# Optimization experiments

Measured on AMD Instinct MI355X. Metric: run time of the kernel, lower is better.

Reference implementation:

```python
import jax, jax.numpy as jnp
import numpy as np

B, V, F = 64, 4096, 16
A, P, NF = 8, 16, 16  # n_aggregators, n_propagate, n_filters


def setup_inputs() -> dict:
    key = jax.random.key(0)
    ks = jax.random.split(key, 6)
    data = jax.random.normal(ks[0], (B, V, F), dtype=jnp.float32)
    num_vertex = jax.random.randint(ks[1], (B, 1), 1, V + 1, dtype=jnp.int32)
    W_flr = jax.random.normal(ks[2], (F, P), dtype=jnp.float32) * (1.0 / np.sqrt(F))
    b_flr = jnp.zeros((P,), jnp.float32)
    W_s = jax.random.normal(ks[3], (F, A), dtype=jnp.float32) * (1.0 / np.sqrt(F))
    b_s = jnp.zeros((A,), jnp.float32)
    W_out = jax.random.normal(ks[4], (A * P, NF), dtype=jnp.float32) * (1.0 / np.sqrt(A * P))
    b_out = jnp.zeros((NF,), jnp.float32)
    return {"data": data, "num_vertex": num_vertex, "W_flr": W_flr, "b_flr": b_flr,
            "W_s": W_s, "b_s": b_s, "W_out": W_out, "b_out": b_out}


def reference(data, num_vertex, W_flr, b_flr, W_s, b_s, W_out, b_out):
    # vertex mask: [B, V, 1], 1.0 where index < num_vertex
    idx = jnp.arange(V, dtype=jnp.int32)[None, :]          # [1, V]
    mask = (idx < num_vertex).astype(jnp.float32)[..., None]  # [B, V, 1]

    features = data @ W_flr + b_flr                         # [B, V, P]
    distance = data @ W_s + b_s                             # [B, V, A]
    edge_weights = mask * jnp.exp(-jnp.square(distance))    # [B, V, A]

    # aggregated mean over vertices: mean_v(ew[b,v,a] * feat[b,v,p]) -> [B, A, P]
    aggregated = jnp.einsum('bva,bvp->bap', edge_weights, features) / V

    # broadcast back: ew[b,v,a] * agg[b,a,p] -> [B, V, A, P] -> [B, V, A*P]
    updated = (edge_weights[:, :, :, None] * aggregated[:, None, :, :]).reshape(B, V, A * P)

    out = mask * (updated @ W_out + b_out)                  # [B, V, NF], linear activation
    return out
```

## Files before the change

### kernel.cpp

```cpp
#include <hip/hip_runtime.h>


#define B_ 64
#define V_ 4096
#define F_ 16
#define A_ 8
#define P_ 16
#define NF_ 16
#define SPLIT1 8
#define SPLIT2 16
#define GE_ (A_*F_ + A_)
#define CH_ 34

typedef unsigned int uint32;
typedef unsigned short u16;

__device__ __forceinline__ float bflo(uint32 u){ union{uint32 i;float f;}x; x.i=u<<16; return x.f; }
__device__ __forceinline__ float bfhi(uint32 u){ union{uint32 i;float f;}x; x.i=u&0xffff0000u; return x.f; }

__device__ __forceinline__ bool detect_bf16(const void* data){
  const uint32* w = (const uint32*)data;
  int c = 0;
  #pragma unroll
  for (int i=0;i<16;++i){
    uint32 e = (w[i]>>7) & 0xffu;
    c += (e>=100u && e<=135u) ? 1 : 0;
  }
  return c >= 11;
}

template<bool BF16>
__device__ __forceinline__ float ldw(const void* p, int i){
  return BF16 ? bflo((uint32)((const u16*)p)[i]) : ((const float*)p)[i];
}

template<bool BF16>
__device__ __forceinline__ void load_vertex(const void* base, size_t v, float* d){
  if (BF16){
    const uint4* p = (const uint4*)((const u16*)base + v*F_);
    uint4 r0=p[0], r1=p[1];
    d[0]=bflo(r0.x); d[1]=bfhi(r0.x); d[2]=bflo(r0.y); d[3]=bfhi(r0.y);
    d[4]=bflo(r0.z); d[5]=bfhi(r0.z); d[6]=bflo(r0.w); d[7]=bfhi(r0.w);
    d[8]=bflo(r1.x); d[9]=bfhi(r1.x); d[10]=bflo(r1.y); d[11]=bfhi(r1.y);
    d[12]=bflo(r1.z); d[13]=bfhi(r1.z); d[14]=bflo(r1.w); d[15]=bfhi(r1.w);
  } else {
    const float4* p = (const float4*)((const float*)base + v*F_);
    float4 a=p[0], b=p[1], c=p[2], e=p[3];
    d[0]=a.x; d[1]=a.y; d[2]=a.z; d[3]=a.w;
    d[4]=b.x; d[5]=b.y; d[6]=b.z; d[7]=b.w;
    d[8]=c.x; d[9]=c.y; d[10]=c.z; d[11]=c.w;
    d[12]=e.x; d[13]=e.y; d[14]=e.z; d[15]=e.w;
  }
}

template<bool BF16>
__device__ __forceinline__ void agg_body(
    const void* __restrict__ data, const int* __restrict__ nv,
    const void* __restrict__ Ws, const void* __restrict__ bs,
    float* __restrict__ partial)
{
  __shared__ __align__(16) float sWs[F_*A_];
  __shared__ float sbs[A_];
  __shared__ float red[256][CH_+1];
  __shared__ float red2[4][CH_];

  const int tid = threadIdx.x;
  if (tid < F_*A_) sWs[tid] = ldw<BF16>(Ws, tid);
  if (tid < A_)    sbs[tid] = ldw<BF16>(bs, tid);
  const int b = blockIdx.x >> 3;
  const int s = blockIdx.x & 7;
  const int nvb = nv[b];
  __syncthreads();

  float G[A_*F_], E[A_];
  #pragma unroll
  for (int i=0;i<A_*F_;++i) G[i]=0.f;
  #pragma unroll
  for (int i=0;i<A_;++i) E[i]=0.f;

  const int vbase = s*(V_/SPLIT1);
  const size_t voff = (size_t)b*V_ + vbase;

  const int vl0 = tid, vl1 = tid + 256;
  float d0[16], d1[16];
  load_vertex<BF16>(data, voff+vl0, d0);
  load_vertex<BF16>(data, voff+vl1, d1);
  const float m0 = (vbase+vl0 < nvb) ? 1.f : 0.f;
  const float m1 = (vbase+vl1 < nvb) ? 1.f : 0.f;

  float t0[A_], t1[A_];
  #pragma unroll
  for (int a=0;a<A_;++a){ t0[a]=sbs[a]; t1[a]=sbs[a]; }
  #pragma unroll
  for (int f=0; f<F_; ++f){
    const float4 w0 = *(const float4*)&sWs[f*A_];
    const float4 w1 = *(const float4*)&sWs[f*A_+4];
    const float wa[8] = {w0.x,w0.y,w0.z,w0.w,w1.x,w1.y,w1.z,w1.w};
    #pragma unroll
    for (int a=0;a<A_;++a){
      t0[a] = fmaf(d0[f], wa[a], t0[a]);
      t1[a] = fmaf(d1[f], wa[a], t1[a]);
    }
  }
  #pragma unroll
  for (int a=0;a<A_;++a){
    const float e0 = m0*__expf(-t0[a]*t0[a]);
    const float e1 = m1*__expf(-t1[a]*t1[a]);
    E[a] = e0+e1;
    #pragma unroll
    for (int f=0;f<F_;++f)
      G[a*F_+f] = fmaf(e0, d0[f], e1*d1[f]);
  }

  #pragma unroll
  for (int c=0;c<4;++c){
    #pragma unroll
    for (int j=0;j<CH_;++j){
      const int idx = c*CH_ + j;
      red[tid][j] = (idx < A_*F_) ? G[idx] : E[idx - A_*F_];
    }
    __syncthreads();
    if (tid < 4*CH_){
      const int j = tid >> 2, q = tid & 3;
      float acc = 0.f;
      #pragma unroll 8
      for (int i=0;i<64;++i) acc += red[64*q + i][j];
      red2[q][j] = acc;
    }
    __syncthreads();
    if (tid < CH_)
      partial[(size_t)blockIdx.x*GE_ + c*CH_ + tid] =
          red2[0][tid]+red2[1][tid]+red2[2][tid]+red2[3][tid];
    __syncthreads();
  }
}

__global__ __launch_bounds__(256, 2) void k_agg(
    const void* __restrict__ data, const int* __restrict__ nv,
    const void* __restrict__ Ws, const void* __restrict__ bs,
    float* __restrict__ partial)
{
  if (detect_bf16(data)) agg_body<true >(data, nv, Ws, bs, partial);
  else                   agg_body<false>(data, nv, Ws, bs, partial);
}

template<bool BF16>
__device__ __forceinline__ void out_body(
    const void* __restrict__ data, const int* __restrict__ nv,
    const void* __restrict__ Wflr, const void* __restrict__ bflr,
    const void* __restrict__ Ws, const void* __restrict__ bs,
    const void* __restrict__ Wout, const void* __restrict__ bout,
    const float* __restrict__ partial, float* __restrict__ out)
{
  __shared__ __align__(16) float sWs[F_*A_];
  __shared__ __align__(16) float sWf[F_*P_];
  __shared__ float sbf[P_], sbs[A_], sbo[NF_];
  __shared__ float sGE[GE_];
  __shared__ float sagg[A_*P_];
  __shared__ __align__(16) float sM[A_*NF_];

  const int tid = threadIdx.x;
  const int b = blockIdx.x >> 4;
  const int s = blockIdx.x & 15;

  if (tid < F_*P_) sWf[tid] = ldw<BF16>(Wflr, tid);
  if (tid < F_*A_) sWs[tid] = ldw<BF16>(Ws, tid);
  if (tid < P_)    sbf[tid] = ldw<BF16>(bflr, tid);
  if (tid < A_)    sbs[tid] = ldw<BF16>(bs, tid);
  if (tid < NF_)   sbo[tid] = ldw<BF16>(bout, tid);
  if (tid < GE_) {
    const float* pp = partial + (size_t)(b*SPLIT1)*GE_ + tid;
    float v = 0.f;
    #pragma unroll
    for (int k=0;k<SPLIT1;++k) v += pp[(size_t)k*GE_];
    sGE[tid] = v;
  }
  const int nvb = nv[b];
  __syncthreads();

  if (tid < A_*P_) {
    const int a = tid >> 4, p = tid & 15;
    float acc = sGE[A_*F_ + a] * sbf[p];
    #pragma unroll
    for (int f=0;f<F_;++f) acc = fmaf(sGE[a*F_+f], sWf[f*P_+p], acc);
    sagg[tid] = acc * (1.0f/(float)V_);
  }
  __syncthreads();
  if (tid < A_*NF_) {
    const int a = tid >> 4, n = tid & 15;
    float m = 0.f;
    #pragma unroll
    for (int p=0;p<P_;++p)
      m = fmaf(sagg[a*P_+p], ldw<BF16>(Wout, (a*P_+p)*NF_+n), m);
    sM[tid] = m;
  }
  __syncthreads();

  const int vbase = s*(V_/SPLIT2);
  const int vl = tid;
  const size_t voff = (size_t)b*V_ + vbase;
  float d0[16];
  load_vertex<BF16>(data, voff+vl, d0);
  const float m = (vbase+vl < nvb) ? 1.f : 0.f;

  float t0[A_];
  #pragma unroll
  for (int a=0;a<A_;++a) t0[a]=sbs[a];
  #pragma unroll
  for (int f=0; f<F_; ++f){
    const float4 w0 = *(const float4*)&sWs[f*A_];
    const float4 w1 = *(const float4*)&sWs[f*A_+4];
    const float wa[8] = {w0.x,w0.y,w0.z,w0.w,w1.x,w1.y,w1.z,w1.w};
    #pragma unroll
    for (int a=0;a<A_;++a) t0[a] = fmaf(d0[f], wa[a], t0[a]);
  }

  float o[NF_];
  #pragma unroll
  for (int n=0;n<NF_;++n) o[n]=sbo[n];
  #pragma unroll
  for (int a=0;a<A_;++a){
    const float e = __expf(-t0[a]*t0[a]);
    const float4 q0 = *(const float4*)&sM[a*NF_];
    const float4 q1 = *(const float4*)&sM[a*NF_+4];
    const float4 q2 = *(const float4*)&sM[a*NF_+8];
    const float4 q3 = *(const float4*)&sM[a*NF_+12];
    const float ma[16] = {q0.x,q0.y,q0.z,q0.w, q1.x,q1.y,q1.z,q1.w,
                          q2.x,q2.y,q2.z,q2.w, q3.x,q3.y,q3.z,q3.w};
    #pragma unroll
    for (int n=0;n<NF_;++n) o[n] = fmaf(e, ma[n], o[n]);
  }

  float4* ob = (float4*)(out + (voff+vl)*NF_);
  ob[0] = make_float4(o[0]*m,  o[1]*m,  o[2]*m,  o[3]*m);
  ob[1] = make_float4(o[4]*m,  o[5]*m,  o[6]*m,  o[7]*m);
  ob[2] = make_float4(o[8]*m,  o[9]*m,  o[10]*m, o[11]*m);
  ob[3] = make_float4(o[12]*m, o[13]*m, o[14]*m, o[15]*m);
}

__global__ __launch_bounds__(256, 4) void k_out(
    const void* __restrict__ data, const int* __restrict__ nv,
    const void* __restrict__ Wflr, const void* __restrict__ bflr,
    const void* __restrict__ Ws, const void* __restrict__ bs,
    const void* __restrict__ Wout, const void* __restrict__ bout,
    const float* __restrict__ partial, float* __restrict__ out)
{
  if (detect_bf16(data))
    out_body<true >(data, nv, Wflr, bflr, Ws, bs, Wout, bout, partial, out);
  else
    out_body<false>(data, nv, Wflr, bflr, Ws, bs, Wout, bout, partial, out);
}

extern "C" void kernel_launch(void* const* d_in, const int* in_sizes, int n_in,
                              void* d_out, int out_size, void* d_ws, size_t ws_size,
                              hipStream_t stream) {
  const void* data = d_in[0];
  const int*  nv   = (const int*)d_in[1];
  const void* Wflr = d_in[2];
  const void* bflr = d_in[3];
  const void* Ws   = d_in[4];
  const void* bs   = d_in[5];
  const void* Wout = d_in[6];
  const void* bout = d_in[7];
  float* out = (float*)d_out;
  float* partial = (float*)d_ws;

  hipLaunchKernelGGL(k_agg, dim3(B_*SPLIT1), dim3(256), 0, stream,
                     data, nv, Ws, bs, partial);
  hipLaunchKernelGGL(k_out, dim3(B_*SPLIT2), dim3(256), 0, stream,
                     data, nv, Wflr, bflr, Ws, bs, Wout, bout, partial, out);
}
```

Before: 99.49 us.

## Restructure aggregation reduction via LDS-staged e and data with per-thread output slices

The aggregation kernel no longer holds a 136-float G accumulator per thread and reduces it through a large padded shared array in four chunked passes. Each thread now stages its edge weights and vertex features into shared memory, and thread groups compute four G outputs over 32-vertex slices before a small cross-group reduction. This cuts register pressure, which allows launch bounds of 4 blocks per CU, and reduces shared-memory traffic. The cost is extra barriers per tile and a less regular final reduction.

```diff
diff --git a/kernel.cpp b/kernel.cpp
--- a/kernel.cpp
+++ b/kernel.cpp
@@ -10,7 +10,8 @@
 #define SPLIT1 8
 #define SPLIT2 16
 #define GE_ (A_*F_ + A_)
-#define CH_ 34
+#define ESTR 12
+#define DSTR 20
 
 typedef unsigned int uint32;
 typedef unsigned short u16;
@@ -61,8 +62,10 @@
 {
   __shared__ __align__(16) float sWs[F_*A_];
   __shared__ float sbs[A_];
-  __shared__ float red[256][CH_+1];
-  __shared__ float red2[4][CH_];
+  __shared__ __align__(16) float e_lds[256*ESTR];
+  __shared__ __align__(16) float d_lds[256*DSTR];
+  __shared__ __align__(16) float gred[8*32*4];
+  __shared__ float ered2[16*8];
 
   const int tid = threadIdx.x;
   if (tid < F_*A_) sWs[tid] = ldw<BF16>(Ws, tid);
@@ -72,70 +75,97 @@
   const int nvb = nv[b];
   __syncthreads();
 
-  float G[A_*F_], E[A_];
-  #pragma unroll
-  for (int i=0;i<A_*F_;++i) G[i]=0.f;
-  #pragma unroll
-  for (int i=0;i<A_;++i) E[i]=0.f;
-
   const int vbase = s*(V_/SPLIT1);
   const size_t voff = (size_t)b*V_ + vbase;
 
-  const int vl0 = tid, vl1 = tid + 256;
-  float d0[16], d1[16];
-  load_vertex<BF16>(data, voff+vl0, d0);
-  load_vertex<BF16>(data, voff+vl1, d1);
-  const float m0 = (vbase+vl0 < nvb) ? 1.f : 0.f;
-  const float m1 = (vbase+vl1 < nvb) ? 1.f : 0.f;
-
-  float t0[A_], t1[A_];
-  #pragma unroll
-  for (int a=0;a<A_;++a){ t0[a]=sbs[a]; t1[a]=sbs[a]; }
-  #pragma unroll
-  for (int f=0; f<F_; ++f){
-    const float4 w0 = *(const float4*)&sWs[f*A_];
-    const float4 w1 = *(const float4*)&sWs[f*A_+4];
-    const float wa[8] = {w0.x,w0.y,w0.z,w0.w,w1.x,w1.y,w1.z,w1.w};
+  const int g  = tid & 31;
+  const int c  = tid >> 5;
+  const int ga = g >> 2;
+  const int gf = g & 3;
+
+  float acc0=0.f, acc1=0.f, acc2=0.f, acc3=0.f;
+  float E[A_];
+  #pragma unroll
+  for (int a=0;a<A_;++a) E[a]=0.f;
+
+  #pragma unroll
+  for (int T=0; T<2; ++T) {
+    const int vl = T*256 + tid;
+    float d0[16];
+    load_vertex<BF16>(data, voff+vl, d0);
+    const float m = (vbase+vl < nvb) ? 1.f : 0.f;
+
+    float t0[A_];
+    #pragma unroll
+    for (int a=0;a<A_;++a) t0[a]=sbs[a];
+    #pragma unroll
+    for (int f=0; f<F_; ++f){
+      const float4 w0 = *(const float4*)&sWs[f*A_];
+      const float4 w1 = *(const float4*)&sWs[f*A_+4];
+      const float wa[8] = {w0.x,w0.y,w0.z,w0.w,w1.x,w1.y,w1.z,w1.w};
+      #pragma unroll
+      for (int a=0;a<A_;++a) t0[a] = fmaf(d0[f], wa[a], t0[a]);
+    }
+    float e0[A_];
     #pragma unroll
     for (int a=0;a<A_;++a){
-      t0[a] = fmaf(d0[f], wa[a], t0[a]);
-      t1[a] = fmaf(d1[f], wa[a], t1[a]);
+      e0[a] = m*__expf(-t0[a]*t0[a]);
+      E[a] += e0[a];
     }
-  }
-  #pragma unroll
-  for (int a=0;a<A_;++a){
-    const float e0 = m0*__expf(-t0[a]*t0[a]);
-    const float e1 = m1*__expf(-t1[a]*t1[a]);
-    E[a] = e0+e1;
-    #pragma unroll
-    for (int f=0;f<F_;++f)
-      G[a*F_+f] = fmaf(e0, d0[f], e1*d1[f]);
-  }
-
-  #pragma unroll
-  for (int c=0;c<4;++c){
-    #pragma unroll
-    for (int j=0;j<CH_;++j){
-      const int idx = c*CH_ + j;
-      red[tid][j] = (idx < A_*F_) ? G[idx] : E[idx - A_*F_];
+    float* er = &e_lds[tid*ESTR];
+    *(float4*)(er)   = make_float4(e0[0],e0[1],e0[2],e0[3]);
+    *(float4*)(er+4) = make_float4(e0[4],e0[5],e0[6],e0[7]);
+    float* dr = &d_lds[tid*DSTR];
+    *(float4*)(dr)    = make_float4(d0[0],d0[1],d0[2],d0[3]);
+    *(float4*)(dr+4)  = make_float4(d0[4],d0[5],d0[6],d0[7]);
+    *(float4*)(dr+8)  = make_float4(d0[8],d0[9],d0[10],d0[11]);
+    *(float4*)(dr+12) = make_float4(d0[12],d0[13],d0[14],d0[15]);
+    __syncthreads();
+
+    const float* ep = &e_lds[(c<<5)*ESTR + ga];
+    const float* dp = &d_lds[(c<<5)*DSTR + gf*4];
+    #pragma unroll 8
+    for (int i=0;i<32;++i){
+      const float e  = ep[i*ESTR];
+      const float4 dv = *(const float4*)(dp + i*DSTR);
+      acc0 = fmaf(e, dv.x, acc0);
+      acc1 = fmaf(e, dv.y, acc1);
+      acc2 = fmaf(e, dv.z, acc2);
+      acc3 = fmaf(e, dv.w, acc3);
     }
     __syncthreads();
-    if (tid < 4*CH_){
-      const int j = tid >> 2, q = tid & 3;
-      float acc = 0.f;
-      #pragma unroll 8
-      for (int i=0;i<64;++i) acc += red[64*q + i][j];
-      red2[q][j] = acc;
-    }
-    __syncthreads();
-    if (tid < CH_)
-      partial[(size_t)blockIdx.x*GE_ + c*CH_ + tid] =
-          red2[0][tid]+red2[1][tid]+red2[2][tid]+red2[3][tid];
-    __syncthreads();
-  }
-}
-
-__global__ __launch_bounds__(256, 2) void k_agg(
+  }
+
+  *(float4*)&gred[(c*32+g)*4] = make_float4(acc0,acc1,acc2,acc3);
+  float* er = &e_lds[tid*ESTR];
+  *(float4*)(er)   = make_float4(E[0],E[1],E[2],E[3]);
+  *(float4*)(er+4) = make_float4(E[4],E[5],E[6],E[7]);
+  __syncthreads();
+
+  if (tid < 128){
+    const int gg = tid >> 2, fi = tid & 3;
+    float sum = 0.f;
+    #pragma unroll
+    for (int k=0;k<8;++k) sum += gred[(k*32+gg)*4 + fi];
+    partial[(size_t)blockIdx.x*GE_ + (gg>>2)*F_ + (gg&3)*4 + fi] = sum;
+  } else {
+    const int t2 = tid - 128;
+    const int q = t2 >> 3, a = t2 & 7;
+    float sum = 0.f;
+    #pragma unroll
+    for (int i=0;i<16;++i) sum += e_lds[(q*16+i)*ESTR + a];
+    ered2[q*8 + a] = sum;
+  }
+  __syncthreads();
+  if (tid < A_){
+    float sum = 0.f;
+    #pragma unroll
+    for (int q=0;q<16;++q) sum += ered2[q*8 + tid];
+    partial[(size_t)blockIdx.x*GE_ + A_*F_ + tid] = sum;
+  }
+}
+
+__global__ __launch_bounds__(256, 4) void k_agg(
     const void* __restrict__ data, const int* __restrict__ nv,
     const void* __restrict__ Ws, const void* __restrict__ bs,
     float* __restrict__ partial)
```

New measurement: 96.60 us. -2.9%, faster.
